# Kernel tuning notes

Hardware: AMD Instinct MI355X
Metric: run time of the kernel (lower is better)

Reference implementation:

```python
import jax, jax.numpy as jnp
import numpy as np

N = 50000      # nodes
E = 800000     # edges
D_IN, D_HID, D_OUT = 1433, 64, 7
EPS = 1e-7       # eps[float32] in hgcn Hyperboloid
MIN_NORM = 1e-15
MAX_NORM = 1e6
# c = 1 -> K = 1/c = 1, sqrtK = 1 (folded into constants below)


def proj(x):
    # reset time coordinate so point lies on the hyperboloid
    y = x[:, 1:]
    y_sqnorm = jnp.sum(y * y, axis=1, keepdims=True)
    x0 = jnp.sqrt(jnp.clip(1.0 + y_sqnorm, EPS))
    return jnp.concatenate([x0, y], axis=1)


def proj_tan0(u):
    return jnp.concatenate([jnp.zeros_like(u[:, :1]), u[:, 1:]], axis=1)


def expmap0(u):
    x = u[:, 1:]
    x_norm = jnp.clip(jnp.linalg.norm(x, axis=1, keepdims=True), MIN_NORM)
    theta = x_norm
    res = jnp.concatenate([jnp.cosh(theta), jnp.sinh(theta) * x / x_norm], axis=1)
    return proj(res)


def logmap0(x):
    y = x[:, 1:]
    y_norm = jnp.clip(jnp.linalg.norm(y, axis=1, keepdims=True), MIN_NORM)
    theta = jnp.clip(x[:, :1], 1.0 + EPS)
    return jnp.concatenate([jnp.zeros_like(theta), jnp.arccosh(theta) * y / y_norm], axis=1)


def minkowski_dot(x, y):
    return jnp.sum(x * y, axis=-1, keepdims=True) - 2.0 * x[:, :1] * y[:, :1]


def proj_tan(u, x):
    ux = jnp.sum(x[:, 1:] * u[:, 1:], axis=1, keepdims=True)
    v0 = ux / jnp.clip(x[:, :1], EPS)
    return jnp.concatenate([v0, u[:, 1:]], axis=1)


def expmap(u, x):
    normu = jnp.sqrt(jnp.clip(minkowski_dot(u, u), EPS))
    normu = jnp.minimum(normu, MAX_NORM)
    theta = jnp.clip(normu, MIN_NORM)
    result = jnp.cosh(theta) * x + jnp.sinh(theta) * u / theta
    return proj(result)


def ptransp0(x, u):
    x0, y = x[:, :1], x[:, 1:]
    y_norm = jnp.clip(jnp.linalg.norm(y, axis=1, keepdims=True), MIN_NORM)
    yn = y / y_norm
    v = jnp.concatenate([-y_norm, (1.0 - x0) * yn], axis=1)
    alpha = jnp.sum(yn * u[:, 1:], axis=1, keepdims=True)
    return proj_tan(u - alpha * v, x)


def mobius_add(x, y):
    u = logmap0(y)
    v = ptransp0(x, u)
    return expmap(v, x)


def hyp_linear(x, W, b):
    # mobius_matvec then hyperbolic bias add (dropout=0)
    mv = expmap0(logmap0(x) @ W.T)
    res = proj(mv)
    hyp_bias = proj(expmap0(proj_tan0(b[None, :])))
    return proj(mobius_add(res, hyp_bias))


def hyp_agg(x, row, col, edge_weight):
    # spmm(adj, logmap0(x)) via edge-list scatter-add
    xt = logmap0(x)
    msg = edge_weight[:, None] * xt[col]          # [E, d]
    support = jax.ops.segment_sum(msg, row, num_segments=N)
    return proj(expmap0(support))


def hyp_act(x):
    xt = jax.nn.relu(logmap0(x))
    xt = proj_tan0(xt)
    return proj(expmap0(xt))


def setup_inputs() -> dict:
    key = jax.random.key(0)
    ks = jax.random.split(key, 8)
    return {
        "x": jax.random.normal(ks[0], (N, D_IN), dtype=jnp.float32),
        "row": jax.random.randint(ks[1], (E,), 0, N),
        "col": jax.random.randint(ks[2], (E,), 0, N),
        "edge_weight": jax.random.uniform(ks[3], (E,), dtype=jnp.float32) * 0.1,
        "W1": jax.random.normal(ks[4], (D_HID, D_IN), dtype=jnp.float32) * 0.02,
        "b1": jax.random.normal(ks[5], (D_HID,), dtype=jnp.float32) * 0.02,
        "W2": jax.random.normal(ks[6], (D_OUT, D_HID), dtype=jnp.float32) * 0.05,
        "b2": jax.random.normal(ks[7], (D_OUT,), dtype=jnp.float32) * 0.02,
    }


def reference(x, row, col, edge_weight, W1, b1, W2, b2):
    # map features to the hyperboloid
    x_hyp = proj(expmap0(proj_tan0(x)))
    # layer 1: HypLinear -> HypAgg -> HypAct
    h = hyp_act(hyp_agg(hyp_linear(x_hyp, W1, b1), row, col, edge_weight))
    # layer 2
    h = hyp_act(hyp_agg(hyp_linear(h, W2, b2), row, col, edge_weight))
    # back to tangent space at origin
    return proj_tan0(logmap0(h))
```

## Files before the change

kernel.cpp:

```cpp
#include <hip/hip_runtime.h>
#include <hip/hip_bf16.h>

#define NN 50000
#define EE 800000
#define DIN 1433
#define KTOT 1432
#define KHALF 716
#define NKT 23
#define NB 196
#define EPSC 1e-7f
#define MINN 1e-15f
#define MAXN 1e6f

typedef __attribute__((ext_vector_type(8))) short bf16x8;
typedef __attribute__((ext_vector_type(4))) float f32x4;

#define WF_OFF     0
#define Z1A_OFF    94208
#define Z1B_OFF    (Z1A_OFF + 3200000)
#define XT3_OFF    (Z1B_OFF + 3200000)
#define CNT_OFF    (XT3_OFF + 400000)
#define ROWPTR_OFF (CNT_OFF + 50000)
#define CUR_OFF    (ROWPTR_OFF + 50002)
#define BSUM_OFF   (CUR_OFF + 50000)
#define BOFF_OFF   (BSUM_OFF + 256)
#define UB_OFF     (BOFF_OFF + 256)
#define EP_OFF     (UB_OFF + 128)

__device__ __forceinline__ float wsum(float v) {
#pragma unroll
  for (int o = 1; o < 64; o <<= 1) v += __shfl_xor(v, o, 64);
  return v;
}

__device__ __forceinline__ float gsum8(float v) {
#pragma unroll
  for (int o = 1; o < 8; o <<= 1) v += __shfl_xor(v, o, 64);
  return v;
}

__device__ __forceinline__ void split_bf(float v, unsigned int& hbits16, unsigned int& lbits16) {
  unsigned int b = __float_as_uint(v);
  unsigned int hb = b & 0xFFFF0000u;
  float r = v - __uint_as_float(hb);
  unsigned int lb = __float_as_uint(r);
  lbits16 = (lb + 0x7FFFu + ((lb >> 16) & 1u)) >> 16;
  hbits16 = hb >> 16;
}

__device__ __forceinline__ float fsinh(float x) {
  float e = __expf(x);
  return 0.5f * (e - __fdividef(1.f, e));
}
__device__ __forceinline__ float facoshp(float z) {
  return __logf(z + sqrtf(fmaxf(z * z - 1.f, 0.f)));
}

__device__ float bias_tangent(const float* b, int lane, int D) {
  const bool sp = (lane >= 1) && (lane < D);
  float bsp = sp ? b[lane] : 0.f;
  float rb = fmaxf(sqrtf(wsum(bsp * bsp)), MINN);
  float bsh = fsinh(rb);
  float hb = sp ? bsh * __fdividef(bsp, rb) : 0.f;
  float hbn2 = wsum(hb * hb);
  float hb0 = sqrtf(fmaxf(1.f + hbn2, EPSC));
  float hbyn = fmaxf(sqrtf(hbn2), MINN);
  return sp ? facoshp(fmaxf(hb0, 1.f + EPSC)) * __fdividef(hb, hbyn) : 0.f;
}

__device__ float chain_with_u(float z, float u, int lane, int D) {
  const bool sp = (lane >= 1) && (lane < D);
  float s = sp ? z : 0.f;
  float r = fmaxf(sqrtf(wsum(s * s)), MINN);
  float sh = fsinh(r);
  float y = sp ? sh * __fdividef(s, r) : 0.f;
  float yn2 = wsum(y * y);
  float x0 = sqrtf(fmaxf(1.f + yn2, EPSC));
  float y_norm = fmaxf(sqrtf(yn2), MINN);
  float ynv = sp ? __fdividef(y, y_norm) : 0.f;
  float alpha = wsum(ynv * u);
  float wsp = sp ? u - alpha * (1.f - x0) * ynv : 0.f;
  float ux = wsum(y * wsp);
  float v0 = __fdividef(ux, fmaxf(x0, EPSC));
  float vt = (lane == 0) ? v0 : wsp;
  float md = wsum(vt * vt) - 2.f * v0 * v0;
  float nu = sqrtf(fmaxf(md, EPSC));
  nu = fminf(nu, MAXN);
  float th = fmaxf(nu, MINN);
  float e = __expf(th), ei = __fdividef(1.f, e);
  float cth = 0.5f * (e + ei), sth = 0.5f * (e - ei);
  float resx = (lane == 0) ? x0 : y;
  float eres = fmaf(cth, resx, sth * __fdividef(vt, th));
  float en2 = wsum(sp ? eres * eres : 0.f);
  float e0 = sqrtf(fmaxf(1.f + en2, EPSC));
  float eyn = fmaxf(sqrtf(en2), MINN);
  return sp ? facoshp(fmaxf(e0, 1.f + EPSC)) * __fdividef(eres, eyn) : 0.f;
}

__device__ float agg_act_chain(float sin_, int lane, int D) {
  const bool sp = (lane >= 1) && (lane < D);
  float s = sp ? sin_ : 0.f;
  float r = fmaxf(sqrtf(wsum(s * s)), MINN);
  float sh = fsinh(r);
  float g = sp ? sh * __fdividef(s, r) : 0.f;
  float gn2 = wsum(g * g);
  float g0 = sqrtf(fmaxf(1.f + gn2, EPSC));
  float gyn = fmaxf(sqrtf(gn2), MINN);
  float l = sp ? facoshp(fmaxf(g0, 1.f + EPSC)) * __fdividef(g, gyn) : 0.f;
  float t = fmaxf(l, 0.f);
  float rt = fmaxf(sqrtf(wsum(t * t)), MINN);
  float sht = fsinh(rt);
  float h = sp ? sht * __fdividef(t, rt) : 0.f;
  float hn2 = wsum(h * h);
  float h0 = sqrtf(fmaxf(1.f + hn2, EPSC));
  float hyn = fmaxf(sqrtf(hn2), MINN);
  return sp ? facoshp(fmaxf(h0, 1.f + EPSC)) * __fdividef(h, hyn) : 0.f;
}

__device__ float agg_act_chain8(float sin_, int f) {
  const bool sp = (f >= 1) && (f < 7);
  float s = sp ? sin_ : 0.f;
  float r = fmaxf(sqrtf(gsum8(s * s)), MINN);
  float sh = fsinh(r);
  float g = sp ? sh * __fdividef(s, r) : 0.f;
  float gn2 = gsum8(g * g);
  float g0 = sqrtf(fmaxf(1.f + gn2, EPSC));
  float gyn = fmaxf(sqrtf(gn2), MINN);
  float l = sp ? facoshp(fmaxf(g0, 1.f + EPSC)) * __fdividef(g, gyn) : 0.f;
  float t = fmaxf(l, 0.f);
  float rt = fmaxf(sqrtf(gsum8(t * t)), MINN);
  float sht = fsinh(rt);
  float h = sp ? sht * __fdividef(t, rt) : 0.f;
  float hn2 = gsum8(h * h);
  float h0 = sqrtf(fmaxf(1.f + hn2, EPSC));
  float hyn = fmaxf(sqrtf(hn2), MINN);
  return sp ? facoshp(fmaxf(h0, 1.f + EPSC)) * __fdividef(h, hyn) : 0.f;
}

__global__ __launch_bounds__(256) void prep_wb_zero(const float* __restrict__ W1,
                                                    const float* __restrict__ b1,
                                                    const float* __restrict__ b2,
                                                    unsigned short* __restrict__ wfrag,
                                                    float* __restrict__ ub,
                                                    int* __restrict__ cnt) {
  if (blockIdx.x >= 93) {
    int i = (blockIdx.x - 93) * 256 + threadIdx.x;
    if (i < NN) cnt[i] = 0;
    return;
  }
  if (blockIdx.x == 92) {
    const int w = threadIdx.x >> 6, lane = threadIdx.x & 63;
    if (w == 0) ub[lane] = bias_tangent(b1, lane, 64);
    else if (w == 1) ub[64 + lane] = bias_tangent(b2, lane, 7);
    return;
  }
  int idx = blockIdx.x * 256 + threadIdx.x;
  int lane = idx & 63;
  int c = (idx >> 6) & 7;
  int rest = idx >> 9;
  int kt = rest % NKT;
  int half = rest / NKT;
  int type = c >> 2, nt = c & 3;
  int col = nt * 16 + (lane & 15);
  unsigned short vals[8];
#pragma unroll
  for (int i = 0; i < 8; ++i) {
    int lk = kt * 32 + (lane >> 4) * 8 + i;
    float wv = (lk < KHALF) ? W1[col * DIN + half * KHALF + lk + 1] : 0.f;
    unsigned int h16, l16;
    split_bf(wv, h16, l16);
    vals[i] = (unsigned short)((type == 0) ? h16 : l16);
  }
  unsigned short* dst = wfrag + (((size_t)(half * NKT + kt) * 8 + c) * 64 + lane) * 8;
#pragma unroll
  for (int i = 0; i < 8; ++i) dst[i] = vals[i];
}

__global__ __launch_bounds__(256) void k_hist(const int* __restrict__ row, int* __restrict__ cnt) {
  int e = blockIdx.x * 256 + threadIdx.x;
  if (e < EE) atomicAdd(&cnt[row[e]], 1);
}

__global__ __launch_bounds__(256) void k_blocksum(const int* __restrict__ cnt,
                                                  int* __restrict__ bsum) {
  __shared__ int wpart[4];
  int i = blockIdx.x * 256 + threadIdx.x;
  int v = (i < NN) ? cnt[i] : 0;
  int s = v;
#pragma unroll
  for (int o = 1; o < 64; o <<= 1) s += __shfl_xor(s, o, 64);
  if ((threadIdx.x & 63) == 0) wpart[threadIdx.x >> 6] = s;
  __syncthreads();
  if (threadIdx.x == 0) bsum[blockIdx.x] = wpart[0] + wpart[1] + wpart[2] + wpart[3];
}

__global__ __launch_bounds__(256) void k_scanb(const int* __restrict__ bsum,
                                               int* __restrict__ boff) {
  __shared__ int s[256];
  int t = threadIdx.x;
  int v = (t < NB) ? bsum[t] : 0;
  s[t] = v;
  __syncthreads();
  for (int o = 1; o < 256; o <<= 1) {
    int a = (t >= o) ? s[t - o] : 0;
    __syncthreads();
    s[t] += a;
    __syncthreads();
  }
  if (t < NB) boff[t] = s[t] - v;
}

__global__ __launch_bounds__(256) void k_apply(const int* __restrict__ cnt,
                                               const int* __restrict__ boff,
                                               int* __restrict__ rowptr, int* __restrict__ cur) {
  __shared__ int s[256];
  int i = blockIdx.x * 256 + threadIdx.x;
  int t = threadIdx.x;
  int v = (i < NN) ? cnt[i] : 0;
  s[t] = v;
  __syncthreads();
  for (int o = 1; o < 256; o <<= 1) {
    int a = (t >= o) ? s[t - o] : 0;
    __syncthreads();
    s[t] += a;
    __syncthreads();
  }
  int ex = s[t] - v + boff[blockIdx.x];
  if (i < NN) { rowptr[i] = ex; cur[i] = ex; }
  if (i == NN - 1) rowptr[NN] = EE;
}

__global__ __launch_bounds__(256) void k_scatter(const int* __restrict__ row,
                                                 const int* __restrict__ col,
                                                 const float* __restrict__ ew,
                                                 int* __restrict__ cur, uint2* __restrict__ ep) {
  int e = blockIdx.x * 256 + threadIdx.x;
  if (e < EE) {
    int p = atomicAdd(&cur[row[e]], 1);
    uint2 q;
    q.x = (unsigned int)col[e];
    q.y = __float_as_uint(ew[e]);
    ep[p] = q;
  }
}

__global__ __launch_bounds__(256) void gemm_half(const float* __restrict__ x,
                                                 const unsigned short* __restrict__ wfrag,
                                                 float* __restrict__ z) {
  __shared__ __align__(16) float XA[3 * 1024];
  __shared__ __align__(16) unsigned short BB[2][8][64][8];
  const int tid = threadIdx.x;
  const int w = tid >> 6, lane = tid & 63;
  const int row0 = blockIdx.x * 32;
  const int half = blockIdx.y;
  const unsigned short* wf = wfrag + (size_t)half * NKT * 4096;
  float* zp = z + (size_t)half * 3200000;
  const int nt0 = (w >> 1) * 2;

  auto stageB = [&](int kt, int p) {
    const unsigned short* src = wf + (size_t)kt * 4096 + (2 * w) * 512 + lane * 8;
    __builtin_amdgcn_global_load_lds(
        (const __attribute__((address_space(1))) unsigned int*)src,
        (__attribute__((address_space(3))) unsigned int*)(&BB[p][2 * w][0][0]), 16, 0, 0);
    __builtin_amdgcn_global_load_lds(
        (const __attribute__((address_space(1))) unsigned int*)(src + 512),
        (__attribute__((address_space(3))) unsigned int*)(&BB[p][2 * w + 1][0][0]), 16, 0, 0);
  };
  auto stageA = [&](int kt, int q) {
    const int r = w * 8 + (lane >> 3);
    const int lb = (lane & 7) ^ (r & 7);
    int grow = row0 + r; if (grow >= NN) grow = NN - 1;
    size_t off = (size_t)grow * DIN + 1 + half * KHALF + kt * 32 + lb * 4;
    if (off > (size_t)NN * DIN - 4) off = (size_t)NN * DIN - 4;
    __builtin_amdgcn_global_load_lds(
        (const __attribute__((address_space(1))) unsigned int*)(x + off),
        (__attribute__((address_space(3))) unsigned int*)(XA + q * 1024 + w * 256),
        16, 0, 0);
  };

  f32x4 acc[2];
  acc[0] = (f32x4){0.f, 0.f, 0.f, 0.f};
  acc[1] = (f32x4){0.f, 0.f, 0.f, 0.f};

  stageB(0, 0);
  stageA(0, 0);
  stageA(1, 1);
  __builtin_amdgcn_sched_barrier(0);
  asm volatile("s_waitcnt vmcnt(1)" ::: "memory");
  __builtin_amdgcn_s_barrier();
  __builtin_amdgcn_sched_barrier(0);

  const int rr = (w & 1) * 16 + (lane & 15);
  const int b0 = (lane >> 4) * 2;
  const int pb0 = (b0 ^ (rr & 7)) * 4;
  const int pb1 = ((b0 + 1) ^ (rr & 7)) * 4;

  for (int kt = 0; kt < NKT; ++kt) {
    if (kt + 1 < NKT) stageB(kt + 1, (kt + 1) & 1);
    if (kt + 2 < NKT) stageA(kt + 2, (kt + 2) % 3);
    const float* xa = XA + (kt % 3) * 1024 + rr * 32;
    float4 f0 = *(const float4*)(xa + pb0);
    float4 f1 = *(const float4*)(xa + pb1);
    float af[8] = {f0.x, f0.y, f0.z, f0.w, f1.x, f1.y, f1.z, f1.w};
    unsigned int h[8], l[8];
#pragma unroll
    for (int j = 0; j < 8; ++j) split_bf(af[j], h[j], l[j]);
    bf16x8 ah, al;
#pragma unroll
    for (int j = 0; j < 8; ++j) { ah[j] = (short)h[j]; al[j] = (short)l[j]; }
    bf16x8 bh[2], bl[2];
#pragma unroll
    for (int n = 0; n < 2; ++n) {
      bh[n] = *(const bf16x8*)&BB[kt & 1][nt0 + n][lane][0];
      bl[n] = *(const bf16x8*)&BB[kt & 1][4 + nt0 + n][lane][0];
    }
    __builtin_amdgcn_s_setprio(1);
#pragma unroll
    for (int n = 0; n < 2; ++n) {
      acc[n] = __builtin_amdgcn_mfma_f32_16x16x32_bf16(ah, bh[n], acc[n], 0, 0, 0);
      acc[n] = __builtin_amdgcn_mfma_f32_16x16x32_bf16(ah, bl[n], acc[n], 0, 0, 0);
      acc[n] = __builtin_amdgcn_mfma_f32_16x16x32_bf16(al, bh[n], acc[n], 0, 0, 0);
    }
    __builtin_amdgcn_s_setprio(0);
    if (kt + 1 < NKT) {
      __builtin_amdgcn_sched_barrier(0);
      asm volatile("s_waitcnt lgkmcnt(0)" ::: "memory");
      if (kt + 2 < NKT) asm volatile("s_waitcnt vmcnt(1)" ::: "memory");
      else              asm volatile("s_waitcnt vmcnt(0)" ::: "memory");
      __builtin_amdgcn_s_barrier();
      __builtin_amdgcn_sched_barrier(0);
    }
  }
#pragma unroll
  for (int n = 0; n < 2; ++n)
#pragma unroll
    for (int i = 0; i < 4; ++i) {
      int orow = row0 + (w & 1) * 16 + (lane >> 4) * 4 + i;
      int ocol = (nt0 + n) * 16 + (lane & 15);
      if (orow < NN) zp[(size_t)orow * 64 + ocol] = acc[n][i];
    }
}

__global__ __launch_bounds__(256) void node1(const float* __restrict__ z1a,
                                             const float* __restrict__ z1b,
                                             const float* __restrict__ ub, float* xt) {
  const int node = blockIdx.x * 4 + (threadIdx.x >> 6);
  const int lane = threadIdx.x & 63;
  const int idx = node * 64 + lane;
  float z = z1a[idx] + z1b[idx];
  float u1 = ub[lane];
  float o = chain_with_u(z, u1, lane, 64);
  xt[idx] = o;
}

__global__ __launch_bounds__(256) void agg1_node2(const int* __restrict__ rowptr,
                                                  const uint2* __restrict__ ep,
                                                  const float* __restrict__ xt,
                                                  const float* __restrict__ W2,
                                                  const float* __restrict__ ub,
                                                  float* __restrict__ xt3) {
  const int node = blockIdx.x * 4 + (threadIdx.x >> 6);
  const int lane = threadIdx.x & 63;
  const int s0 = rowptr[node], s1 = rowptr[node + 1];
  float a0 = 0.f, a1 = 0.f, a2 = 0.f, a3 = 0.f;
  float a4 = 0.f, a5 = 0.f, a6 = 0.f, a7 = 0.f;
  int p = s0;
  for (; p + 8 <= s1; p += 8) {
    uint2 q0 = ep[p], q1 = ep[p + 1], q2 = ep[p + 2], q3 = ep[p + 3];
    uint2 q4 = ep[p + 4], q5 = ep[p + 5], q6 = ep[p + 6], q7 = ep[p + 7];
    a0 = fmaf(__uint_as_float(q0.y), xt[(size_t)q0.x * 64 + lane], a0);
    a1 = fmaf(__uint_as_float(q1.y), xt[(size_t)q1.x * 64 + lane], a1);
    a2 = fmaf(__uint_as_float(q2.y), xt[(size_t)q2.x * 64 + lane], a2);
    a3 = fmaf(__uint_as_float(q3.y), xt[(size_t)q3.x * 64 + lane], a3);
    a4 = fmaf(__uint_as_float(q4.y), xt[(size_t)q4.x * 64 + lane], a4);
    a5 = fmaf(__uint_as_float(q5.y), xt[(size_t)q5.x * 64 + lane], a5);
    a6 = fmaf(__uint_as_float(q6.y), xt[(size_t)q6.x * 64 + lane], a6);
    a7 = fmaf(__uint_as_float(q7.y), xt[(size_t)q7.x * 64 + lane], a7);
  }
  for (; p < s1; ++p) {
    uint2 q = ep[p];
    a0 = fmaf(__uint_as_float(q.y), xt[(size_t)q.x * 64 + lane], a0);
  }
  float acc = ((a0 + a1) + (a2 + a3)) + ((a4 + a5) + (a6 + a7));
  float xt2 = agg_act_chain(acc, lane, 64);
  float z2 = 0.f;
#pragma unroll
  for (int jj = 1; jj < 7; ++jj) {
    float wv = W2[jj * 64 + lane];
    float sjj = wsum(xt2 * wv);
    if (lane == jj) z2 = sjj;
  }
  float u2 = ub[64 + lane];
  float o = chain_with_u(z2, u2, lane, 7);
  if (lane < 8) xt3[node * 8 + lane] = o;
}

__global__ __launch_bounds__(256) void agg2_final(const int* __restrict__ rowptr,
                                                  const uint2* __restrict__ ep,
                                                  const float* __restrict__ xt3,
                                                  float* __restrict__ out) {
  const int node = blockIdx.x * 32 + (threadIdx.x >> 3);
  const int f = threadIdx.x & 7;
  const int nc = (node < NN) ? node : (NN - 1);
  const int s0 = rowptr[nc], s1 = rowptr[nc + 1];
  float a0 = 0.f, a1 = 0.f, a2 = 0.f, a3 = 0.f;
  int p = s0;
  for (; p + 4 <= s1; p += 4) {
    uint2 q0 = ep[p], q1 = ep[p + 1], q2 = ep[p + 2], q3 = ep[p + 3];
    a0 = fmaf(__uint_as_float(q0.y), xt3[(size_t)q0.x * 8 + f], a0);
    a1 = fmaf(__uint_as_float(q1.y), xt3[(size_t)q1.x * 8 + f], a1);
    a2 = fmaf(__uint_as_float(q2.y), xt3[(size_t)q2.x * 8 + f], a2);
    a3 = fmaf(__uint_as_float(q3.y), xt3[(size_t)q3.x * 8 + f], a3);
  }
  for (; p < s1; ++p) {
    uint2 q = ep[p];
    a0 = fmaf(__uint_as_float(q.y), xt3[(size_t)q.x * 8 + f], a0);
  }
  float acc = (a0 + a1) + (a2 + a3);
  float o = agg_act_chain8(acc, f);
  if (node < NN && f < 7) out[node * 7 + f] = o;
}

extern "C" void kernel_launch(void* const* d_in, const int* in_sizes, int n_in,
                              void* d_out, int out_size, void* d_ws, size_t ws_size,
                              hipStream_t stream) {
  const float* x = (const float*)d_in[0];
  const int* row = (const int*)d_in[1];
  const int* col = (const int*)d_in[2];
  const float* ew = (const float*)d_in[3];
  const float* W1 = (const float*)d_in[4];
  const float* b1 = (const float*)d_in[5];
  const float* W2 = (const float*)d_in[6];
  const float* b2 = (const float*)d_in[7];
  float* ws = (float*)d_ws;
  unsigned short* wfrag = (unsigned short*)(ws + WF_OFF);
  float* z1a = ws + Z1A_OFF;
  float* z1b = ws + Z1B_OFF;
  float* xt3 = ws + XT3_OFF;
  int* cnt = (int*)(ws + CNT_OFF);
  int* rowptr = (int*)(ws + ROWPTR_OFF);
  int* cur = (int*)(ws + CUR_OFF);
  int* bsum = (int*)(ws + BSUM_OFF);
  int* boff = (int*)(ws + BOFF_OFF);
  float* ub = ws + UB_OFF;
  uint2* ep = (uint2*)(ws + EP_OFF);
  float* out = (float*)d_out;

  prep_wb_zero<<<dim3(289), dim3(256), 0, stream>>>(W1, b1, b2, wfrag, ub, cnt);

  k_hist<<<dim3(3125), dim3(256), 0, stream>>>(row, cnt);
  k_blocksum<<<dim3(NB), dim3(256), 0, stream>>>(cnt, bsum);
  k_scanb<<<dim3(1), dim3(256), 0, stream>>>(bsum, boff);
  k_apply<<<dim3(NB), dim3(256), 0, stream>>>(cnt, boff, rowptr, cur);
  k_scatter<<<dim3(3125), dim3(256), 0, stream>>>(row, col, ew, cur, ep);

  gemm_half<<<dim3(1563, 2), dim3(256), 0, stream>>>(x, wfrag, z1a);
  node1<<<dim3(12500), dim3(256), 0, stream>>>(z1a, z1b, ub, z1a);

  agg1_node2<<<dim3(12500), dim3(256), 0, stream>>>(rowptr, ep, z1a, W2, ub, xt3);
  agg2_final<<<dim3(1563), dim3(256), 0, stream>>>(rowptr, ep, xt3, out);
}
```

Baseline: 302.8 us.

## Fuse full-K GEMM with node1 epilogue, dropping split-K halves

The GEMM no longer splits K across two blocks in y. Each block now iterates over the whole K range (46 tiles) and applies the hyperbolic node1 chain in an epilogue staged through shared memory. This removes the separate node1 launch and the write and re-read of two 50000x64 partial buffers. In exchange the grid has half as many blocks, so there is less parallelism and each block runs a longer serial K loop.

New measurement: 316.9 us. +4.7%, slower.

```diff
diff --git a/kernel.cpp b/kernel.cpp
--- a/kernel.cpp
+++ b/kernel.cpp
@@ -7,6 +7,7 @@
 #define KTOT 1432
 #define KHALF 716
 #define NKT 23
+#define NKT2 46
 #define NB 196
 #define EPSC 1e-7f
 #define MINN 1e-15f
@@ -16,9 +17,8 @@
 typedef __attribute__((ext_vector_type(4))) float f32x4;
 
 #define WF_OFF     0
-#define Z1A_OFF    94208
-#define Z1B_OFF    (Z1A_OFF + 3200000)
-#define XT3_OFF    (Z1B_OFF + 3200000)
+#define XT_OFF     94208
+#define XT3_OFF    (XT_OFF + 3200000)
 #define CNT_OFF    (XT3_OFF + 400000)
 #define ROWPTR_OFF (CNT_OFF + 50000)
 #define CUR_OFF    (ROWPTR_OFF + 50002)
@@ -244,21 +244,20 @@
   }
 }
 
-__global__ __launch_bounds__(256) void gemm_half(const float* __restrict__ x,
-                                                 const unsigned short* __restrict__ wfrag,
-                                                 float* __restrict__ z) {
+__global__ __launch_bounds__(256) void gemm_node1(const float* __restrict__ x,
+                                                  const unsigned short* __restrict__ wfrag,
+                                                  const float* __restrict__ ub,
+                                                  float* __restrict__ xt) {
   __shared__ __align__(16) float XA[3 * 1024];
   __shared__ __align__(16) unsigned short BB[2][8][64][8];
+  float (*zbuf)[68] = (float (*)[68])XA;
   const int tid = threadIdx.x;
   const int w = tid >> 6, lane = tid & 63;
   const int row0 = blockIdx.x * 32;
-  const int half = blockIdx.y;
-  const unsigned short* wf = wfrag + (size_t)half * NKT * 4096;
-  float* zp = z + (size_t)half * 3200000;
   const int nt0 = (w >> 1) * 2;
 
   auto stageB = [&](int kt, int p) {
-    const unsigned short* src = wf + (size_t)kt * 4096 + (2 * w) * 512 + lane * 8;
+    const unsigned short* src = wfrag + (size_t)kt * 4096 + (2 * w) * 512 + lane * 8;
     __builtin_amdgcn_global_load_lds(
         (const __attribute__((address_space(1))) unsigned int*)src,
         (__attribute__((address_space(3))) unsigned int*)(&BB[p][2 * w][0][0]), 16, 0, 0);
@@ -269,8 +268,9 @@
   auto stageA = [&](int kt, int q) {
     const int r = w * 8 + (lane >> 3);
     const int lb = (lane & 7) ^ (r & 7);
+    const int kb = (kt < NKT) ? kt * 32 : KHALF + (kt - NKT) * 32;
     int grow = row0 + r; if (grow >= NN) grow = NN - 1;
-    size_t off = (size_t)grow * DIN + 1 + half * KHALF + kt * 32 + lb * 4;
+    size_t off = (size_t)grow * DIN + 1 + kb + lb * 4;
     if (off > (size_t)NN * DIN - 4) off = (size_t)NN * DIN - 4;
     __builtin_amdgcn_global_load_lds(
         (const __attribute__((address_space(1))) unsigned int*)(x + off),
@@ -295,9 +295,9 @@
   const int pb0 = (b0 ^ (rr & 7)) * 4;
   const int pb1 = ((b0 + 1) ^ (rr & 7)) * 4;
 
-  for (int kt = 0; kt < NKT; ++kt) {
-    if (kt + 1 < NKT) stageB(kt + 1, (kt + 1) & 1);
-    if (kt + 2 < NKT) stageA(kt + 2, (kt + 2) % 3);
+  for (int kt = 0; kt < NKT2; ++kt) {
+    if (kt + 1 < NKT2) stageB(kt + 1, (kt + 1) & 1);
+    if (kt + 2 < NKT2) stageA(kt + 2, (kt + 2) % 3);
     const float* xa = XA + (kt % 3) * 1024 + rr * 32;
     float4 f0 = *(const float4*)(xa + pb0);
     float4 f1 = *(const float4*)(xa + pb1);
@@ -322,35 +322,32 @@
       acc[n] = __builtin_amdgcn_mfma_f32_16x16x32_bf16(al, bh[n], acc[n], 0, 0, 0);
     }
     __builtin_amdgcn_s_setprio(0);
-    if (kt + 1 < NKT) {
+    if (kt + 1 < NKT2) {
       __builtin_amdgcn_sched_barrier(0);
       asm volatile("s_waitcnt lgkmcnt(0)" ::: "memory");
-      if (kt + 2 < NKT) asm volatile("s_waitcnt vmcnt(1)" ::: "memory");
-      else              asm volatile("s_waitcnt vmcnt(0)" ::: "memory");
+      if (kt + 2 < NKT2) asm volatile("s_waitcnt vmcnt(1)" ::: "memory");
+      else               asm volatile("s_waitcnt vmcnt(0)" ::: "memory");
       __builtin_amdgcn_s_barrier();
       __builtin_amdgcn_sched_barrier(0);
     }
   }
+  __syncthreads();
 #pragma unroll
   for (int n = 0; n < 2; ++n)
 #pragma unroll
     for (int i = 0; i < 4; ++i) {
-      int orow = row0 + (w & 1) * 16 + (lane >> 4) * 4 + i;
-      int ocol = (nt0 + n) * 16 + (lane & 15);
-      if (orow < NN) zp[(size_t)orow * 64 + ocol] = acc[n][i];
+      int r = (w & 1) * 16 + (lane >> 4) * 4 + i;
+      zbuf[r][(nt0 + n) * 16 + (lane & 15)] = acc[n][i];
     }
-}
-
-__global__ __launch_bounds__(256) void node1(const float* __restrict__ z1a,
-                                             const float* __restrict__ z1b,
-                                             const float* __restrict__ ub, float* xt) {
-  const int node = blockIdx.x * 4 + (threadIdx.x >> 6);
-  const int lane = threadIdx.x & 63;
-  const int idx = node * 64 + lane;
-  float z = z1a[idx] + z1b[idx];
+  __syncthreads();
   float u1 = ub[lane];
-  float o = chain_with_u(z, u1, lane, 64);
-  xt[idx] = o;
+  for (int nr = 0; nr < 8; ++nr) {
+    int r = w * 8 + nr;
+    float zv = zbuf[r][lane];
+    float o = chain_with_u(zv, u1, lane, 64);
+    int g = row0 + r;
+    if (g < NN) xt[(size_t)g * 64 + lane] = o;
+  }
 }
 
 __global__ __launch_bounds__(256) void agg1_node2(const int* __restrict__ rowptr,
@@ -434,8 +431,7 @@
   const float* b2 = (const float*)d_in[7];
   float* ws = (float*)d_ws;
   unsigned short* wfrag = (unsigned short*)(ws + WF_OFF);
-  float* z1a = ws + Z1A_OFF;
-  float* z1b = ws + Z1B_OFF;
+  float* xt = ws + XT_OFF;
   float* xt3 = ws + XT3_OFF;
   int* cnt = (int*)(ws + CNT_OFF);
   int* rowptr = (int*)(ws + ROWPTR_OFF);
@@ -454,9 +450,8 @@
   k_apply<<<dim3(NB), dim3(256), 0, stream>>>(cnt, boff, rowptr, cur);
   k_scatter<<<dim3(3125), dim3(256), 0, stream>>>(row, col, ew, cur, ep);
 
-  gemm_half<<<dim3(1563, 2), dim3(256), 0, stream>>>(x, wfrag, z1a);
-  node1<<<dim3(12500), dim3(256), 0, stream>>>(z1a, z1b, ub, z1a);
-
-  agg1_node2<<<dim3(12500), dim3(256), 0, stream>>>(rowptr, ep, z1a, W2, ub, xt3);
+  gemm_node1<<<dim3(1563), dim3(256), 0, stream>>>(x, wfrag, ub, xt);
+
+  agg1_node2<<<dim3(12500), dim3(256), 0, stream>>>(rowptr, ep, xt, W2, ub, xt3);
   agg2_final<<<dim3(1563), dim3(256), 0, stream>>>(rowptr, ep, xt3, out);
 }
```
